# Kernel tuning notes

Measured on AMD Instinct MI355X. Metric: run time of the kernel, lower is better.

Reference implementation:

```python
import jax, jax.numpy as jnp
import numpy as np

N, H, E, P = 100000, 64, 1600000, 3


def setup_inputs() -> dict:
    key = jax.random.key(0)
    ks = jax.random.split(key, 12)
    h = jax.random.normal(ks[0], (N, H), dtype=jnp.float32)
    W = jax.random.normal(ks[1], (P, H, H), dtype=jnp.float32) * 0.1
    b = jnp.zeros((P, H), dtype=jnp.float32)
    a = jnp.full((P,), 0.25, dtype=jnp.float32)  # PReLU slopes (torch default init)
    fc_w = jax.random.normal(ks[2], (H, H), dtype=jnp.float32) * 0.1
    fc_b = jnp.zeros((H,), dtype=jnp.float32)
    att = jax.random.normal(ks[3], (H,), dtype=jnp.float32) * 0.1
    adj_vals = jax.random.uniform(ks[4], (E,), dtype=jnp.float32) * (1.0 / 16.0)
    row = jax.random.randint(ks[5], (E,), 0, N, dtype=jnp.int32)
    col = jax.random.randint(ks[6], (E,), 0, N, dtype=jnp.int32)
    mask1 = jax.random.randint(ks[7], (N,), 0, 2, dtype=jnp.int32).astype(bool)
    mask2 = jax.random.randint(ks[8], (N,), 0, 2, dtype=jnp.int32).astype(bool)
    return {"h": h, "W": W, "b": b, "a": a, "fc_w": fc_w, "fc_b": fc_b,
            "att": att, "adj_vals": adj_vals, "row": row, "col": col,
            "mask1": mask1, "mask2": mask2}


def reference(h, W, b, a, fc_w, fc_b, att, adj_vals, row, col, mask1, mask2):
    n = h.shape[0]

    def gcn_all(x):
        # P GCN layers (small fixed P): linear -> spmm(adj) -> +bias -> PReLU
        outs = []
        for p in range(W.shape[0]):
            fts = x @ W[p].T                                   # [N,H]
            msg = fts[col] * adj_vals[:, None]                  # [E,H] gather
            agg = jax.ops.segment_sum(msg, row, num_segments=n) # [N,H] scatter-add
            o = agg + b[p]
            outs.append(jnp.where(o > 0, o, a[p] * o))          # PReLU
        return jnp.stack(outs)                                  # [P,N,H]

    def attention(embeds):
        # sp_p = mean_n tanh(fc(embed_p)); beta = softmax_p(att . sp_p)
        s = jnp.tanh(jnp.einsum('pnh,kh->pnk', embeds, fc_w) + fc_b).mean(axis=1)  # [P,H]
        beta = jax.nn.softmax(s @ att, axis=0)                                      # [P]
        return jnp.einsum('pnh,p->nh', embeds, beta)                                # [N,H]

    h_masked = h * (~mask1)[:, None].astype(h.dtype)
    z_mp = attention(gcn_all(h_masked))       # encode with mask_ratio1
    z_mp2 = attention(gcn_all(h))             # encode with mask_ratio 0
    z_masked = z_mp * (~mask2)[:, None].astype(h.dtype)
    x_recon = attention(gcn_all(z_masked))    # decode
    return (z_mp, z_mp2, x_recon)
```

## Files before the change

kernel.cpp:

```cpp
#include <hip/hip_runtime.h>
#include <hip/hip_bf16.h>

typedef __hip_bfloat16 bf16;
typedef __attribute__((ext_vector_type(8))) short bf16x8;
typedef __attribute__((ext_vector_type(4))) float f32x4;


__device__ __forceinline__ short f2bf(float x) {
    unsigned u = __float_as_uint(x);
    unsigned r = (u + 0x7FFFu + ((u >> 16) & 1u)) >> 16;
    return (short)r;
}
__device__ __forceinline__ float bf2f(short s) {
    return __uint_as_float(((unsigned)(unsigned short)s) << 16);
}
__device__ __forceinline__ void split1(float v, short& h, short& l) {
    h = f2bf(v);
    l = f2bf(v - bf2f(h));
}
__device__ __forceinline__ void split1_rtz(float v, short& h, short& l) {
    unsigned u = __float_as_uint(v);
    h = (short)(u >> 16);
    float r = v - __uint_as_float(u & 0xFFFF0000u);
    l = f2bf(r);
}

__device__ __forceinline__ float fast_tanh(float x) {
    float t = __expf(x + x);
    return 1.f - __fdividef(2.f, t + 1.f);
}

__device__ __forceinline__ void fma4(float4& acc, float v, const float4& x) {
    acc.x = fmaf(v, x.x, acc.x);
    acc.y = fmaf(v, x.y, acc.y);
    acc.z = fmaf(v, x.z, acc.z);
    acc.w = fmaf(v, x.w, acc.w);
}

__device__ __forceinline__ void red4(float4& a) {
    a.x += __shfl_xor(a.x, 16); a.y += __shfl_xor(a.y, 16);
    a.z += __shfl_xor(a.z, 16); a.w += __shfl_xor(a.w, 16);
    a.x += __shfl_xor(a.x, 32); a.y += __shfl_xor(a.y, 32);
    a.z += __shfl_xor(a.z, 32); a.w += __shfl_xor(a.w, 32);
}

__global__ __launch_bounds__(256) void forensic_kernel(const unsigned int* __restrict__ mask_w,
                                                       const unsigned int* __restrict__ idx_w,
                                                       int nw_mask, int nw_idx,
                                                       int* __restrict__ flags) {
    __shared__ int sm[6];
    int t = threadIdx.x;
    if (t < 6) sm[t] = 0;
    __syncthreads();
    int m_gt1 = 0, m_f32 = 0, m_f64 = 0, m_oddnz = 0, i_hi = 0, i_oddnz = 0;
    for (int i = t; i < nw_mask; i += 256) {
        unsigned int w = mask_w[i];
        if (w > 1u && w != 0x3F800000u && w != 0x3FF00000u) m_gt1++;
        if (w == 0x3F800000u) m_f32++;
        if ((i & 1) && w == 0x3FF00000u) m_f64++;
        if ((i & 1) && w != 0u) m_oddnz++;
    }
    for (int i = t; i < nw_idx; i += 256) {
        unsigned int v = idx_w[i];
        if (v >= 0x20000000u) i_hi++;
        if ((i & 1) && v != 0u) i_oddnz++;
    }
    atomicAdd(&sm[0], m_gt1);
    atomicAdd(&sm[1], m_f32);
    atomicAdd(&sm[2], m_f64);
    atomicAdd(&sm[3], m_oddnz);
    atomicAdd(&sm[4], i_hi);
    atomicAdd(&sm[5], i_oddnz);
    __syncthreads();
    if (t == 0) {
        int mmode;
        if (sm[1] > 50) mmode = 2;
        else if (sm[2] > 50) mmode = 4;
        else if (sm[0] > 50) mmode = 0;
        else if (sm[3] > 50) mmode = 1;
        else mmode = 3;
        int imode;
        if (sm[4] > (nw_idx * 3) / 4) imode = 2;
        else if (sm[4] > nw_idx / 4) imode = 4;
        else if (sm[5] > 50) imode = 1;
        else imode = 3;
        flags[0] = mmode;
        flags[1] = imode;
    }
}

__device__ __forceinline__ int fetch_idx(const void* p, int e, int mode) {
    switch (mode) {
        case 1: return ((const int*)p)[e];
        case 3: return (int)(((const long long*)p)[e]);
        case 2: return (int)(((const float*)p)[e]);
        default: return (int)(((const double*)p)[e]);
    }
}

__device__ __forceinline__ bool conv_one(const void* m, int mode, int i) {
    switch (mode) {
        case 0: return ((const unsigned char*)m)[i] != 0;
        case 1: return ((const int*)m)[i] != 0;
        case 2: return ((const float*)m)[i] != 0.f;
        case 3: return ((const long long*)m)[i] != 0;
        default: return ((const double*)m)[i] != 0.0;
    }
}

__global__ __launch_bounds__(256) void conv_masks(const void* __restrict__ m1,
                                                  const void* __restrict__ m2,
                                                  const int* __restrict__ flags, int n,
                                                  unsigned char* __restrict__ o1,
                                                  unsigned char* __restrict__ o2) {
    int mode = flags[0];
    int i = blockIdx.x * 256 + threadIdx.x;
    if (i >= n) return;
    o1[i] = conv_one(m1, mode, i) ? 1 : 0;
    o2[i] = conv_one(m2, mode, i) ? 1 : 0;
}


__global__ __launch_bounds__(256) void split_weights(const float* __restrict__ W,
                                                     const float* __restrict__ fcw, int wn,
                                                     int fn, short* __restrict__ whi,
                                                     short* __restrict__ wlo,
                                                     short* __restrict__ fhi,
                                                     short* __restrict__ flo) {
    int i = blockIdx.x * 256 + threadIdx.x;
    if (i < wn) {
        short h, l;
        split1(W[i], h, l);
        whi[i] = h;
        wlo[i] = l;
    } else if (i < wn + fn) {
        int j = i - wn;
        short h, l;
        split1(fcw[j], h, l);
        fhi[j] = h;
        flo[j] = l;
    }
}


__global__ __launch_bounds__(256) void bucket_hist(const void* __restrict__ row,
                                                   const int* __restrict__ flags, int e_cnt,
                                                   int n, int shift, int nb,
                                                   int* __restrict__ bcnt) {
    __shared__ int hist[2048];
    int t = threadIdx.x;
    for (int i = t; i < nb; i += 256) hist[i] = 0;
    __syncthreads();
    int imode = flags[1];
    for (int e = blockIdx.x * 256 + t; e < e_cnt; e += gridDim.x * 256) {
        int r = fetch_idx(row, e, imode);
        if ((unsigned)r < (unsigned)n) atomicAdd(&hist[r >> shift], 1);
    }
    __syncthreads();
    for (int i = t; i < nb; i += 256)
        if (hist[i]) atomicAdd(&bcnt[i], hist[i]);
}

__global__ __launch_bounds__(1024) void bucket_scan(int* __restrict__ bptr, int nb,
                                                    int* __restrict__ bcur, int n,
                                                    int* __restrict__ row_ptr) {
    __shared__ int sh[1024];
    int t = threadIdx.x;
    int i0 = t * 2, i1 = t * 2 + 1;
    int a = (i0 < nb) ? bptr[i0] : 0;
    int b = (i1 < nb) ? bptr[i1] : 0;
    int s = a + b;
    sh[t] = s;
    __syncthreads();
    for (int off = 1; off < 1024; off <<= 1) {
        int u = (t >= off) ? sh[t - off] : 0;
        __syncthreads();
        sh[t] += u;
        __syncthreads();
    }
    int base = sh[t] - s;
    if (i0 < nb) { bptr[i0] = base; bcur[i0] = base; }
    if (i1 < nb) { bptr[i1] = base + a; bcur[i1] = base + a; }
    if (t == 1023) {
        bptr[nb] = sh[1023];
        row_ptr[n] = sh[1023];
    }
}

__global__ __launch_bounds__(256) void bin_pass2(const void* __restrict__ row,
                                                 const void* __restrict__ col,
                                                 const float* __restrict__ vals,
                                                 const int* __restrict__ flags, int e_cnt, int n,
                                                 int shift, int nb, int* __restrict__ bcur,
                                                 int2* __restrict__ rcbin,
                                                 float* __restrict__ valbin) {
    __shared__ int hist[2048];
    __shared__ int base[2048];
    int t = threadIdx.x;
    int e0 = blockIdx.x * 2048;
    if (e0 >= e_cnt) return;
    int imode = flags[1];
    for (int i = t; i < nb; i += 256) hist[i] = 0;
    __syncthreads();
    int rr[8], cc[8];
    float vv[8];
    bool ok[8];
#pragma unroll
    for (int j = 0; j < 8; j++) {
        int e = e0 + j * 256 + t;
        ok[j] = false;
        if (e < e_cnt) {
            int r = fetch_idx(row, e, imode);
            if ((unsigned)r < (unsigned)n) {
                ok[j] = true;
                rr[j] = r;
                int c = fetch_idx(col, e, imode);
                cc[j] = ((unsigned)c < (unsigned)n) ? c : 0;
                vv[j] = vals[e];
                atomicAdd(&hist[r >> shift], 1);
            }
        }
    }
    __syncthreads();
    for (int i = t; i < nb; i += 256) {
        int c = hist[i];
        base[i] = c ? atomicAdd(&bcur[i], c) : 0;
        hist[i] = 0;
    }
    __syncthreads();
#pragma unroll
    for (int j = 0; j < 8; j++) {
        if (ok[j]) {
            int bk = rr[j] >> shift;
            int pos = base[bk] + atomicAdd(&hist[bk], 1);
            rcbin[pos] = make_int2(rr[j], cc[j]);
            valbin[pos] = vv[j];
        }
    }
}

__global__ __launch_bounds__(512) void csr_finalize(const int* __restrict__ bptr,
                                                    const int2* __restrict__ rcbin,
                                                    const float* __restrict__ valbin, int n,
                                                    int shift, int* __restrict__ row_ptr,
                                                    int* __restrict__ col_s,
                                                    float* __restrict__ val_s) {
    __shared__ int cnt[1024];
    __shared__ int curs[1024];
    __shared__ int red[512];
    int b = blockIdx.x, t = threadIdx.x;
    int rpb = 1 << shift;
    int r0 = b << shift;
    int rows = n - r0;
    if (rows <= 0) return;
    if (rows > rpb) rows = rpb;
    int ebase = bptr[b], eend = bptr[b + 1];
    for (int i = t; i < rows; i += 512) cnt[i] = 0;
    __syncthreads();
    for (int e = ebase + t; e < eend; e += 512) atomicAdd(&cnt[rcbin[e].x - r0], 1);
    __syncthreads();
    int v[2], s = 0;
#pragma unroll
    for (int j = 0; j < 2; j++) {
        int idx = t * 2 + j;
        v[j] = (idx < rows) ? cnt[idx] : 0;
        s += v[j];
    }
    red[t] = s;
    __syncthreads();
    for (int off = 1; off < 512; off <<= 1) {
        int u = (t >= off) ? red[t - off] : 0;
        __syncthreads();
        red[t] += u;
        __syncthreads();
    }
    int run = ebase + red[t] - s;
#pragma unroll
    for (int j = 0; j < 2; j++) {
        int idx = t * 2 + j;
        if (idx < rows) {
            row_ptr[r0 + idx] = run;
            curs[idx] = run;
            run += v[j];
        }
    }
    __syncthreads();
    for (int e = ebase + t; e < eend; e += 512) {
        int2 rc = rcbin[e];
        float vv = valbin[e];
        int pos = atomicAdd(&curs[rc.x - r0], 1);
        col_s[pos] = rc.y;
        val_s[pos] = vv;
    }
}


__device__ __forceinline__ void store_split4(short* __restrict__ hi, short* __restrict__ lo,
                                             size_t o, const float4& v) {
    short4 h4, l4;
    split1(v.x, h4.x, l4.x); split1(v.y, h4.y, l4.y);
    split1(v.z, h4.z, l4.z); split1(v.w, h4.w, l4.w);
    *(short4*)(hi + o) = h4;
    *(short4*)(lo + o) = l4;
}

__global__ __launch_bounds__(256) void spmm_dual(const float* __restrict__ X,
                                                 const int* __restrict__ row_ptr,
                                                 const int* __restrict__ col_s,
                                                 const float* __restrict__ val_s,
                                                 const unsigned char* __restrict__ mask, int n,
                                                 short* __restrict__ axm_hi,
                                                 short* __restrict__ axm_lo,
                                                 short* __restrict__ axf_hi,
                                                 short* __restrict__ axf_lo) {
    int gid = blockIdx.x * 256 + threadIdx.x;
    int r = gid >> 6;
    if (r >= n) return;
    int lane = threadIdx.x & 63;
    int g = lane >> 4, sub = lane & 15;
    int s = row_ptr[r], e = row_ptr[r + 1];
    int cnt = e - s;
    int mycm = 0;
    float myv = 0.f;
    if (lane < cnt) {
        int c = col_s[s + lane];
        myv = val_s[s + lane];
        mycm = c | (mask[c] ? (1 << 30) : 0);
    }
    int cmain = cnt > 64 ? 64 : cnt;
    float4 fA = {0, 0, 0, 0}, fB = {0, 0, 0, 0};
    float4 dA = {0, 0, 0, 0}, dB = {0, 0, 0, 0};
    for (int i = 0; i < cmain; i += 16) {
        int i0 = i + g, i1 = i + 4 + g, i2 = i + 8 + g, i3 = i + 12 + g;
        int c0 = __shfl(mycm, i0), c1 = __shfl(mycm, i1);
        int c2 = __shfl(mycm, i2), c3 = __shfl(mycm, i3);
        float v0 = __shfl(myv, i0), v1 = __shfl(myv, i1);
        float v2 = __shfl(myv, i2), v3 = __shfl(myv, i3);
        if (i0 < cmain) {
            float4 x = *(const float4*)(X + (size_t)(c0 & 0x3FFFFFFF) * 64 + sub * 4);
            fma4(fA, v0, x);
            if (c0 >> 30) fma4(dA, v0, x);
        }
        if (i1 < cmain) {
            float4 x = *(const float4*)(X + (size_t)(c1 & 0x3FFFFFFF) * 64 + sub * 4);
            fma4(fB, v1, x);
            if (c1 >> 30) fma4(dB, v1, x);
        }
        if (i2 < cmain) {
            float4 x = *(const float4*)(X + (size_t)(c2 & 0x3FFFFFFF) * 64 + sub * 4);
            fma4(fA, v2, x);
            if (c2 >> 30) fma4(dA, v2, x);
        }
        if (i3 < cmain) {
            float4 x = *(const float4*)(X + (size_t)(c3 & 0x3FFFFFFF) * 64 + sub * 4);
            fma4(fB, v3, x);
            if (c3 >> 30) fma4(dB, v3, x);
        }
    }
    for (int i = 64 + g; i < cnt; i += 4) {
        int c = col_s[s + i];
        float v = val_s[s + i];
        float4 x = *(const float4*)(X + (size_t)c * 64 + sub * 4);
        fma4(fA, v, x);
        if (mask[c]) fma4(dA, v, x);
    }
    fA.x += fB.x; fA.y += fB.y; fA.z += fB.z; fA.w += fB.w;
    dA.x += dB.x; dA.y += dB.y; dA.z += dB.z; dA.w += dB.w;
    red4(fA);
    red4(dA);
    if (g == 0) {
        float4 mA = make_float4(fA.x - dA.x, fA.y - dA.y, fA.z - dA.z, fA.w - dA.w);
        size_t o = (size_t)r * 64 + sub * 4;
        store_split4(axf_hi, axf_lo, o, fA);
        store_split4(axm_hi, axm_lo, o, mA);
    }
}

__global__ __launch_bounds__(256) void spmm_one(const float* __restrict__ X,
                                                const int* __restrict__ row_ptr,
                                                const int* __restrict__ col_s,
                                                const float* __restrict__ val_s,
                                                const unsigned char* __restrict__ mask, int n,
                                                short* __restrict__ ax_hi,
                                                short* __restrict__ ax_lo) {
    int gid = blockIdx.x * 256 + threadIdx.x;
    int r = gid >> 6;
    if (r >= n) return;
    int lane = threadIdx.x & 63;
    int g = lane >> 4, sub = lane & 15;
    int s = row_ptr[r], e = row_ptr[r + 1];
    int cnt = e - s;
    int myc = 0;
    float myv = 0.f;
    if (lane < cnt) {
        myc = col_s[s + lane];
        float v = val_s[s + lane];
        myv = mask[myc] ? 0.f : v;
    }
    int cmain = cnt > 64 ? 64 : cnt;
    float4 aA = {0, 0, 0, 0}, aB = {0, 0, 0, 0};
    for (int i = 0; i < cmain; i += 16) {
        int i0 = i + g, i1 = i + 4 + g, i2 = i + 8 + g, i3 = i + 12 + g;
        int c0 = __shfl(myc, i0), c1 = __shfl(myc, i1);
        int c2 = __shfl(myc, i2), c3 = __shfl(myc, i3);
        float v0 = __shfl(myv, i0), v1 = __shfl(myv, i1);
        float v2 = __shfl(myv, i2), v3 = __shfl(myv, i3);
        if (i0 < cmain && v0 != 0.f) {
            float4 x = *(const float4*)(X + (size_t)c0 * 64 + sub * 4);
            fma4(aA, v0, x);
        }
        if (i1 < cmain && v1 != 0.f) {
            float4 x = *(const float4*)(X + (size_t)c1 * 64 + sub * 4);
            fma4(aB, v1, x);
        }
        if (i2 < cmain && v2 != 0.f) {
            float4 x = *(const float4*)(X + (size_t)c2 * 64 + sub * 4);
            fma4(aA, v2, x);
        }
        if (i3 < cmain && v3 != 0.f) {
            float4 x = *(const float4*)(X + (size_t)c3 * 64 + sub * 4);
            fma4(aB, v3, x);
        }
    }
    for (int i = 64 + g; i < cnt; i += 4) {
        int c = col_s[s + i];
        if (mask[c]) continue;
        float v = val_s[s + i];
        float4 x = *(const float4*)(X + (size_t)c * 64 + sub * 4);
        fma4(aA, v, x);
    }
    aA.x += aB.x; aA.y += aB.y; aA.z += aB.z; aA.w += aB.w;
    red4(aA);
    if (g == 0) {
        size_t o = (size_t)r * 64 + sub * 4;
        store_split4(ax_hi, ax_lo, o, aA);
    }
}


template <int PP>
__global__ __launch_bounds__(512) void gemm_tanh(const short* __restrict__ Xhi0,
                                                 const short* __restrict__ Xlo0,
                                                 const short* __restrict__ Xhi1,
                                                 const short* __restrict__ Xlo1,
                                                 const short* __restrict__ Whi_g,
                                                 const short* __restrict__ Wlo_g,
                                                 const float* __restrict__ b,
                                                 const float* __restrict__ a,
                                                 const short* __restrict__ fchi_g,
                                                 const short* __restrict__ fclo_g,
                                                 const float* __restrict__ fcb, int n, int ntiles,
                                                 float* __restrict__ s_sums) {
    __shared__ __align__(16) short ehi[2][PP][16][72], elo[2][PP][16][72];
    int set = blockIdx.y;
    const short* __restrict__ Xhi = set ? Xhi1 : Xhi0;
    const short* __restrict__ Xlo = set ? Xlo1 : Xlo0;
    float* __restrict__ ss = s_sums + set * 512;
    int t = threadIdx.x;
    int grp = t >> 8;
    int wv = (t >> 6) & 3, lane = t & 63, nl = lane & 15, q = lane >> 4;
    int colg = wv * 16 + nl;
    bf16x8 whi[PP][2], wlo[PP][2];
    float bias[PP], slope[PP];
#pragma unroll
    for (int p = 0; p < PP; p++) {
#pragma unroll
        for (int kk = 0; kk < 2; kk++) {
            whi[p][kk] = *(const bf16x8*)(Whi_g + p * 4096 + colg * 64 + kk * 32 + q * 8);
            wlo[p][kk] = *(const bf16x8*)(Wlo_g + p * 4096 + colg * 64 + kk * 32 + q * 8);
        }
        bias[p] = b[p * 64 + colg];
        slope[p] = a[p];
    }
    bf16x8 fhi[2], flo[2];
#pragma unroll
    for (int kk = 0; kk < 2; kk++) {
        fhi[kk] = *(const bf16x8*)(fchi_g + colg * 64 + kk * 32 + q * 8);
        flo[kk] = *(const bf16x8*)(fclo_g + colg * 64 + kk * 32 + q * 8);
    }
    float fbias = fcb[colg];
    float ssum[PP];
#pragma unroll
    for (int p = 0; p < PP; p++) ssum[p] = 0.f;

    int npairs = (ntiles + 1) >> 1;
    int pi = blockIdx.x;
    int rt = pi * 2 + grp;
    bool act = rt < ntiles;
    bf16x8 ah[2], al[2];
    if (act) {
        size_t rb = (size_t)(rt * 16 + nl) * 64 + q * 8;
#pragma unroll
        for (int kk = 0; kk < 2; kk++) {
            ah[kk] = *(const bf16x8*)(Xhi + rb + kk * 32);
            al[kk] = *(const bf16x8*)(Xlo + rb + kk * 32);
        }
    }
    for (; pi < npairs; pi += gridDim.x) {
        rt = pi * 2 + grp;
        act = rt < ntiles;
        if (act) {
#pragma unroll
            for (int p = 0; p < PP; p++) {
                f32x4 acc = {0.f, 0.f, 0.f, 0.f};
                acc = __builtin_amdgcn_mfma_f32_16x16x32_bf16(ah[0], whi[p][0], acc, 0, 0, 0);
                acc = __builtin_amdgcn_mfma_f32_16x16x32_bf16(ah[1], whi[p][1], acc, 0, 0, 0);
                acc = __builtin_amdgcn_mfma_f32_16x16x32_bf16(al[0], whi[p][0], acc, 0, 0, 0);
                acc = __builtin_amdgcn_mfma_f32_16x16x32_bf16(al[1], whi[p][1], acc, 0, 0, 0);
                acc = __builtin_amdgcn_mfma_f32_16x16x32_bf16(ah[0], wlo[p][0], acc, 0, 0, 0);
                acc = __builtin_amdgcn_mfma_f32_16x16x32_bf16(ah[1], wlo[p][1], acc, 0, 0, 0);
                acc = __builtin_amdgcn_mfma_f32_16x16x32_bf16(al[0], wlo[p][0], acc, 0, 0, 0);
                acc = __builtin_amdgcn_mfma_f32_16x16x32_bf16(al[1], wlo[p][1], acc, 0, 0, 0);
#pragma unroll
                for (int i = 0; i < 4; i++) {
                    float o = acc[i] + bias[p];
                    o = (o > 0.f) ? o : slope[p] * o;
                    short hb, lb;
                    split1_rtz(o, hb, lb);
                    ehi[grp][p][q * 4 + i][colg] = hb;
                    elo[grp][p][q * 4 + i][colg] = lb;
                }
            }
        }
        int pn = pi + gridDim.x;
        int rn = pn * 2 + grp;
        bf16x8 pfh[2], pfl[2];
        if (pn < npairs && rn < ntiles) {
            size_t rb = (size_t)(rn * 16 + nl) * 64 + q * 8;
#pragma unroll
            for (int kk = 0; kk < 2; kk++) {
                pfh[kk] = *(const bf16x8*)(Xhi + rb + kk * 32);
                pfl[kk] = *(const bf16x8*)(Xlo + rb + kk * 32);
            }
        }
        __syncthreads();
        if (act) {
#pragma unroll
            for (int p = 0; p < PP; p++) {
                bf16x8 eh[2], el[2];
#pragma unroll
                for (int kk = 0; kk < 2; kk++) {
                    eh[kk] = *(const bf16x8*)(&ehi[grp][p][nl][kk * 32 + q * 8]);
                    el[kk] = *(const bf16x8*)(&elo[grp][p][nl][kk * 32 + q * 8]);
                }
                f32x4 acc = {0.f, 0.f, 0.f, 0.f};
                acc = __builtin_amdgcn_mfma_f32_16x16x32_bf16(eh[0], fhi[0], acc, 0, 0, 0);
                acc = __builtin_amdgcn_mfma_f32_16x16x32_bf16(eh[1], fhi[1], acc, 0, 0, 0);
                acc = __builtin_amdgcn_mfma_f32_16x16x32_bf16(el[0], fhi[0], acc, 0, 0, 0);
                acc = __builtin_amdgcn_mfma_f32_16x16x32_bf16(el[1], fhi[1], acc, 0, 0, 0);
                acc = __builtin_amdgcn_mfma_f32_16x16x32_bf16(eh[0], flo[0], acc, 0, 0, 0);
                acc = __builtin_amdgcn_mfma_f32_16x16x32_bf16(eh[1], flo[1], acc, 0, 0, 0);
#pragma unroll
                for (int i = 0; i < 4; i++) {
                    int r = rt * 16 + q * 4 + i;
                    if (r < n) ssum[p] += fast_tanh(acc[i] + fbias);
                }
            }
        }
        __syncthreads();
#pragma unroll
        for (int kk = 0; kk < 2; kk++) {
            ah[kk] = pfh[kk];
            al[kk] = pfl[kk];
        }
    }
#pragma unroll
    for (int p = 0; p < PP; p++) {
        float s = ssum[p];
        s += __shfl_xor(s, 16);
        s += __shfl_xor(s, 32);
        if (q == 0) atomicAdd(&ss[p * 64 + colg], s);
    }
}


template <int PP>
__global__ __launch_bounds__(256) void gemm_mix(const short* __restrict__ Xhi0,
                                                const short* __restrict__ Xlo0,
                                                const short* __restrict__ Xhi1,
                                                const short* __restrict__ Xlo1,
                                                const short* __restrict__ Whi_g,
                                                const short* __restrict__ Wlo_g,
                                                const float* __restrict__ b,
                                                const float* __restrict__ a,
                                                const float* __restrict__ beta, int n, int ntiles,
                                                float* __restrict__ outbase, int accum) {
    int set = blockIdx.y;
    const short* __restrict__ Xhi = set ? Xhi1 : Xhi0;
    const short* __restrict__ Xlo = set ? Xlo1 : Xlo0;
    float* __restrict__ out = outbase + (size_t)set * n * 64;
    int t = threadIdx.x;
    int wv = t >> 6, lane = t & 63, nl = lane & 15, q = lane >> 4;
    int colg = wv * 16 + nl;
    bf16x8 whi[PP][2], wlo[PP][2];
    float bias[PP], slope[PP], bet[PP];
#pragma unroll
    for (int p = 0; p < PP; p++) {
#pragma unroll
        for (int kk = 0; kk < 2; kk++) {
            whi[p][kk] = *(const bf16x8*)(Whi_g + p * 4096 + colg * 64 + kk * 32 + q * 8);
            wlo[p][kk] = *(const bf16x8*)(Wlo_g + p * 4096 + colg * 64 + kk * 32 + q * 8);
        }
        bias[p] = b[p * 64 + colg];
        slope[p] = a[p];
        bet[p] = beta[set * 8 + p];
    }
    int rt = blockIdx.x;
    bf16x8 ah[2], al[2];
    if (rt < ntiles) {
        size_t rb = (size_t)(rt * 16 + nl) * 64 + q * 8;
#pragma unroll
        for (int kk = 0; kk < 2; kk++) {
            ah[kk] = *(const bf16x8*)(Xhi + rb + kk * 32);
            al[kk] = *(const bf16x8*)(Xlo + rb + kk * 32);
        }
    }
    for (; rt < ntiles; rt += gridDim.x) {
        int rn = rt + gridDim.x;
        bf16x8 pfh[2], pfl[2];
        if (rn < ntiles) {
            size_t rb = (size_t)(rn * 16 + nl) * 64 + q * 8;
#pragma unroll
            for (int kk = 0; kk < 2; kk++) {
                pfh[kk] = *(const bf16x8*)(Xhi + rb + kk * 32);
                pfl[kk] = *(const bf16x8*)(Xlo + rb + kk * 32);
            }
        }
        float mix[4] = {0.f, 0.f, 0.f, 0.f};
#pragma unroll
        for (int p = 0; p < PP; p++) {
            f32x4 acc = {0.f, 0.f, 0.f, 0.f};
            acc = __builtin_amdgcn_mfma_f32_16x16x32_bf16(ah[0], whi[p][0], acc, 0, 0, 0);
            acc = __builtin_amdgcn_mfma_f32_16x16x32_bf16(ah[1], whi[p][1], acc, 0, 0, 0);
            acc = __builtin_amdgcn_mfma_f32_16x16x32_bf16(al[0], whi[p][0], acc, 0, 0, 0);
            acc = __builtin_amdgcn_mfma_f32_16x16x32_bf16(al[1], whi[p][1], acc, 0, 0, 0);
            acc = __builtin_amdgcn_mfma_f32_16x16x32_bf16(ah[0], wlo[p][0], acc, 0, 0, 0);
            acc = __builtin_amdgcn_mfma_f32_16x16x32_bf16(ah[1], wlo[p][1], acc, 0, 0, 0);
            acc = __builtin_amdgcn_mfma_f32_16x16x32_bf16(al[0], wlo[p][0], acc, 0, 0, 0);
            acc = __builtin_amdgcn_mfma_f32_16x16x32_bf16(al[1], wlo[p][1], acc, 0, 0, 0);
#pragma unroll
            for (int i = 0; i < 4; i++) {
                float o = acc[i] + bias[p];
                o = (o > 0.f) ? o : slope[p] * o;
                mix[i] = fmaf(bet[p], o, mix[i]);
            }
        }
#pragma unroll
        for (int i = 0; i < 4; i++) {
            int r = rt * 16 + q * 4 + i;
            if (r < n) {
                size_t idx = (size_t)r * 64 + colg;
                out[idx] = accum ? (out[idx] + mix[i]) : mix[i];
            }
        }
#pragma unroll
        for (int kk = 0; kk < 2; kk++) {
            ah[kk] = pfh[kk];
            al[kk] = pfl[kk];
        }
    }
}

__global__ __launch_bounds__(64) void compute_beta(const float* __restrict__ s_sums,
                                                   const float* __restrict__ att, int n, int P,
                                                   int nsets, float* __restrict__ beta) {
    int lane = threadIdx.x;
    float av = att[lane];
    for (int st = 0; st < nsets; st++) {
        const float* ss = s_sums + st * 512;
        float l[8];
        for (int p = 0; p < P; p++) l[p] = ss[p * 64 + lane] * av;
#pragma unroll
        for (int off = 32; off > 0; off >>= 1)
            for (int p = 0; p < 8; p++)
                if (p < P) l[p] += __shfl_down(l[p], off);
        if (lane == 0) {
            const float inv = 1.0f / (float)n;
            float m = -1e30f;
            for (int p = 0; p < P; p++) {
                l[p] *= inv;
                m = fmaxf(m, l[p]);
            }
            float s = 0.f;
            for (int p = 0; p < P; p++) {
                l[p] = __expf(l[p] - m);
                s += l[p];
            }
            for (int p = 0; p < P; p++) beta[st * 8 + p] = l[p] / s;
        }
    }
}


extern "C" void kernel_launch(void* const* d_in, const int* in_sizes, int n_in,
                              void* d_out, int out_size, void* d_ws, size_t ws_size,
                              hipStream_t stream) {
    const float* h = (const float*)d_in[0];
    const float* W = (const float*)d_in[1];
    const float* b = (const float*)d_in[2];
    const float* a = (const float*)d_in[3];
    const float* fc_w = (const float*)d_in[4];
    const float* fc_b = (const float*)d_in[5];
    const float* att = (const float*)d_in[6];
    const float* adj = (const float*)d_in[7];
    const void* row = d_in[8];
    const void* col = d_in[9];
    const void* mask1 = d_in[10];
    const void* mask2 = d_in[11];
    float* out = (float*)d_out;

    int P = in_sizes[3];
    if (P < 1 || P > 8) P = 3;
    int N = in_sizes[0] / 64;
    int E = in_sizes[7];
    int N16 = (N + 15) & ~15;
    int ntiles = N16 >> 4;

    int shift = 8;
    while (((N >> shift) + 1) > 2048) shift++;
    int NB = (N >> shift) + 1;

    char* w = (char*)d_ws;
    auto alloc = [&](size_t bytes) {
        void* p = (void*)w;
        w += (bytes + 255) & ~(size_t)255;
        return p;
    };
    int* row_ptr = (int*)alloc((size_t)(N + 1) * 4);
    int* col_s = (int*)alloc((size_t)E * 4);
    float* val_s = (float*)alloc((size_t)E * 4);
    int* bptr = (int*)alloc((size_t)(NB + 1) * 4);
    int* bcur = (int*)alloc((size_t)NB * 4);
    int2* rcbin = (int2*)alloc((size_t)E * 8);
    float* valbin = (float*)alloc((size_t)E * 4);
    unsigned char* m1c = (unsigned char*)alloc(N);
    unsigned char* m2c = (unsigned char*)alloc(N);
    short* axm_hi = (short*)alloc((size_t)N16 * 64 * 2);
    short* axm_lo = (short*)alloc((size_t)N16 * 64 * 2);
    short* axf_hi = (short*)alloc((size_t)N16 * 64 * 2);
    short* axf_lo = (short*)alloc((size_t)N16 * 64 * 2);
    short* whi_g = (short*)alloc((size_t)8 * 4096 * 2);
    short* wlo_g = (short*)alloc((size_t)8 * 4096 * 2);
    short* fchi_g = (short*)alloc((size_t)4096 * 2);
    short* fclo_g = (short*)alloc((size_t)4096 * 2);
    float* s_sums = (float*)alloc(2 * 512 * 4);
    float* beta = (float*)alloc(64 * 4);
    int* flags = (int*)alloc(256);

    int nw_mask = N / 4 > 25000 ? 25000 : N / 4;
    int nw_idx = E / 4 > 25000 ? 25000 : E / 4;
    forensic_kernel<<<1, 256, 0, stream>>>((const unsigned int*)mask1, (const unsigned int*)row,
                                           nw_mask, nw_idx, flags);
    conv_masks<<<(N + 255) / 256, 256, 0, stream>>>(mask1, mask2, flags, N, m1c, m2c);
    int wn = P * 4096, fn = 4096;
    split_weights<<<(wn + fn + 255) / 256, 256, 0, stream>>>(W, fc_w, wn, fn, whi_g, wlo_g,
                                                            fchi_g, fclo_g);

    hipMemsetAsync(bptr, 0, (size_t)(NB + 1) * 4, stream);
    if (N16 > N) {
        size_t padoff = (size_t)N * 64, padbytes = (size_t)(N16 - N) * 64 * 2;
        hipMemsetAsync(axm_hi + padoff, 0, padbytes, stream);
        hipMemsetAsync(axm_lo + padoff, 0, padbytes, stream);
        hipMemsetAsync(axf_hi + padoff, 0, padbytes, stream);
        hipMemsetAsync(axf_lo + padoff, 0, padbytes, stream);
    }
    bucket_hist<<<1024, 256, 0, stream>>>(row, flags, E, N, shift, NB, bptr);
    bucket_scan<<<1, 1024, 0, stream>>>(bptr, NB, bcur, N, row_ptr);
    int bin_blocks = (E + 2047) / 2048;
    bin_pass2<<<bin_blocks, 256, 0, stream>>>(row, col, adj, flags, E, N, shift, NB, bcur, rcbin,
                                              valbin);
    csr_finalize<<<NB, 512, 0, stream>>>(bptr, rcbin, valbin, N, shift, row_ptr, col_s, val_s);

    int spmm_grid = (int)(((size_t)N * 64 + 255) / 256);
    int tanh_blocks = 1024;
    int mix_blocks = 1024;

    auto tail = [&](const short* xh0, const short* xl0, const short* xh1, const short* xl1,
                    int nsets, float* dst) {
        hipMemsetAsync(s_sums, 0, 2 * 512 * 4, stream);
        if (P == 3) {
            gemm_tanh<3><<<dim3(tanh_blocks, nsets), 512, 0, stream>>>(
                xh0, xl0, xh1, xl1, whi_g, wlo_g, b, a, fchi_g, fclo_g, fc_b, N, ntiles, s_sums);
        } else {
            for (int p = 0; p < P; p++)
                gemm_tanh<1><<<dim3(tanh_blocks, nsets), 512, 0, stream>>>(
                    xh0, xl0, xh1, xl1, whi_g + p * 4096, wlo_g + p * 4096, b + p * 64, a + p,
                    fchi_g, fclo_g, fc_b, N, ntiles, s_sums + p * 64);
        }
        compute_beta<<<1, 64, 0, stream>>>(s_sums, att, N, P, nsets, beta);
        if (P == 3) {
            gemm_mix<3><<<dim3(mix_blocks, nsets), 256, 0, stream>>>(
                xh0, xl0, xh1, xl1, whi_g, wlo_g, b, a, beta, N, ntiles, dst, 0);
        } else {
            for (int p = 0; p < P; p++)
                gemm_mix<1><<<dim3(mix_blocks, nsets), 256, 0, stream>>>(
                    xh0, xl0, xh1, xl1, whi_g + p * 4096, wlo_g + p * 4096, b + p * 64, a + p,
                    beta + p, N, ntiles, dst, p != 0);
        }
    };

    spmm_dual<<<spmm_grid, 256, 0, stream>>>(h, row_ptr, col_s, val_s, m1c, N, axm_hi, axm_lo,
                                             axf_hi, axf_lo);
    tail(axm_hi, axm_lo, axf_hi, axf_lo, 2, out);
    spmm_one<<<spmm_grid, 256, 0, stream>>>(out, row_ptr, col_s, val_s, m2c, N, axm_hi, axm_lo);
    tail(axm_hi, axm_lo, axm_hi, axm_lo, 1, out + (size_t)2 * N * 64);
}
```

Before: 647.5 us.

## Software-pipeline gemm_tanh with double-buffered LDS and one barrier per tile

After: 573.9 us. 11.4% less time.

```diff
diff --git a/kernel.cpp b/kernel.cpp
--- a/kernel.cpp
+++ b/kernel.cpp
@@ -439,7 +439,7 @@
 
 
 template <int PP>
-__global__ __launch_bounds__(512) void gemm_tanh(const short* __restrict__ Xhi0,
+__global__ __launch_bounds__(256) void gemm_tanh(const short* __restrict__ Xhi0,
                                                  const short* __restrict__ Xlo0,
                                                  const short* __restrict__ Xhi1,
                                                  const short* __restrict__ Xlo1,
@@ -457,8 +457,7 @@
     const short* __restrict__ Xlo = set ? Xlo1 : Xlo0;
     float* __restrict__ ss = s_sums + set * 512;
     int t = threadIdx.x;
-    int grp = t >> 8;
-    int wv = (t >> 6) & 3, lane = t & 63, nl = lane & 15, q = lane >> 4;
+    int wv = t >> 6, lane = t & 63, nl = lane & 15, q = lane >> 4;
     int colg = wv * 16 + nl;
     bf16x8 whi[PP][2], wlo[PP][2];
     float bias[PP], slope[PP];
@@ -483,86 +482,77 @@
 #pragma unroll
     for (int p = 0; p < PP; p++) ssum[p] = 0.f;
 
-    int npairs = (ntiles + 1) >> 1;
-    int pi = blockIdx.x;
-    int rt = pi * 2 + grp;
-    bool act = rt < ntiles;
-    bf16x8 ah[2], al[2];
-    if (act) {
+    int G = gridDim.x;
+    int rt0 = blockIdx.x;
+    if (rt0 >= ntiles) return;
+
+    auto loadA = [&](int rt, bf16x8 xh[2], bf16x8 xl[2]) {
         size_t rb = (size_t)(rt * 16 + nl) * 64 + q * 8;
 #pragma unroll
         for (int kk = 0; kk < 2; kk++) {
-            ah[kk] = *(const bf16x8*)(Xhi + rb + kk * 32);
-            al[kk] = *(const bf16x8*)(Xlo + rb + kk * 32);
-        }
-    }
-    for (; pi < npairs; pi += gridDim.x) {
-        rt = pi * 2 + grp;
-        act = rt < ntiles;
-        if (act) {
-#pragma unroll
-            for (int p = 0; p < PP; p++) {
-                f32x4 acc = {0.f, 0.f, 0.f, 0.f};
-                acc = __builtin_amdgcn_mfma_f32_16x16x32_bf16(ah[0], whi[p][0], acc, 0, 0, 0);
-                acc = __builtin_amdgcn_mfma_f32_16x16x32_bf16(ah[1], whi[p][1], acc, 0, 0, 0);
-                acc = __builtin_amdgcn_mfma_f32_16x16x32_bf16(al[0], whi[p][0], acc, 0, 0, 0);
-                acc = __builtin_amdgcn_mfma_f32_16x16x32_bf16(al[1], whi[p][1], acc, 0, 0, 0);
-                acc = __builtin_amdgcn_mfma_f32_16x16x32_bf16(ah[0], wlo[p][0], acc, 0, 0, 0);
-                acc = __builtin_amdgcn_mfma_f32_16x16x32_bf16(ah[1], wlo[p][1], acc, 0, 0, 0);
-                acc = __builtin_amdgcn_mfma_f32_16x16x32_bf16(al[0], wlo[p][0], acc, 0, 0, 0);
-                acc = __builtin_amdgcn_mfma_f32_16x16x32_bf16(al[1], wlo[p][1], acc, 0, 0, 0);
-#pragma unroll
-                for (int i = 0; i < 4; i++) {
-                    float o = acc[i] + bias[p];
-                    o = (o > 0.f) ? o : slope[p] * o;
-                    short hb, lb;
-                    split1_rtz(o, hb, lb);
-                    ehi[grp][p][q * 4 + i][colg] = hb;
-                    elo[grp][p][q * 4 + i][colg] = lb;
-                }
-            }
-        }
-        int pn = pi + gridDim.x;
-        int rn = pn * 2 + grp;
-        bf16x8 pfh[2], pfl[2];
-        if (pn < npairs && rn < ntiles) {
-            size_t rb = (size_t)(rn * 16 + nl) * 64 + q * 8;
+            xh[kk] = *(const bf16x8*)(Xhi + rb + kk * 32);
+            xl[kk] = *(const bf16x8*)(Xlo + rb + kk * 32);
+        }
+    };
+    auto embed = [&](bf16x8 xh[2], bf16x8 xl[2], int bsel) {
+#pragma unroll
+        for (int p = 0; p < PP; p++) {
+            f32x4 acc = {0.f, 0.f, 0.f, 0.f};
+            acc = __builtin_amdgcn_mfma_f32_16x16x32_bf16(xh[0], whi[p][0], acc, 0, 0, 0);
+            acc = __builtin_amdgcn_mfma_f32_16x16x32_bf16(xh[1], whi[p][1], acc, 0, 0, 0);
+            acc = __builtin_amdgcn_mfma_f32_16x16x32_bf16(xl[0], whi[p][0], acc, 0, 0, 0);
+            acc = __builtin_amdgcn_mfma_f32_16x16x32_bf16(xl[1], whi[p][1], acc, 0, 0, 0);
+            acc = __builtin_amdgcn_mfma_f32_16x16x32_bf16(xh[0], wlo[p][0], acc, 0, 0, 0);
+            acc = __builtin_amdgcn_mfma_f32_16x16x32_bf16(xh[1], wlo[p][1], acc, 0, 0, 0);
+            acc = __builtin_amdgcn_mfma_f32_16x16x32_bf16(xl[0], wlo[p][0], acc, 0, 0, 0);
+            acc = __builtin_amdgcn_mfma_f32_16x16x32_bf16(xl[1], wlo[p][1], acc, 0, 0, 0);
+#pragma unroll
+            for (int i = 0; i < 4; i++) {
+                float o = acc[i] + bias[p];
+                o = (o > 0.f) ? o : slope[p] * o;
+                short hb, lb;
+                split1_rtz(o, hb, lb);
+                ehi[bsel][p][q * 4 + i][colg] = hb;
+                elo[bsel][p][q * 4 + i][colg] = lb;
+            }
+        }
+    };
+
+    bf16x8 ah[2], al[2], pfh[2], pfl[2];
+    loadA(rt0, ah, al);
+    embed(ah, al, 0);
+    if (rt0 + G < ntiles) loadA(rt0 + G, pfh, pfl);
+
+    int buf = 0;
+    for (int rt = rt0; rt < ntiles; rt += G) {
+        int rn = rt + G;
+        __syncthreads();
+        if (rn < ntiles) {
+            embed(pfh, pfl, buf ^ 1);
+            if (rn + G < ntiles) loadA(rn + G, pfh, pfl);
+        }
+#pragma unroll
+        for (int p = 0; p < PP; p++) {
+            bf16x8 eh[2], el[2];
 #pragma unroll
             for (int kk = 0; kk < 2; kk++) {
-                pfh[kk] = *(const bf16x8*)(Xhi + rb + kk * 32);
-                pfl[kk] = *(const bf16x8*)(Xlo + rb + kk * 32);
-            }
-        }
-        __syncthreads();
-        if (act) {
-#pragma unroll
-            for (int p = 0; p < PP; p++) {
-                bf16x8 eh[2], el[2];
-#pragma unroll
-                for (int kk = 0; kk < 2; kk++) {
-                    eh[kk] = *(const bf16x8*)(&ehi[grp][p][nl][kk * 32 + q * 8]);
-                    el[kk] = *(const bf16x8*)(&elo[grp][p][nl][kk * 32 + q * 8]);
-                }
-                f32x4 acc = {0.f, 0.f, 0.f, 0.f};
-                acc = __builtin_amdgcn_mfma_f32_16x16x32_bf16(eh[0], fhi[0], acc, 0, 0, 0);
-                acc = __builtin_amdgcn_mfma_f32_16x16x32_bf16(eh[1], fhi[1], acc, 0, 0, 0);
-                acc = __builtin_amdgcn_mfma_f32_16x16x32_bf16(el[0], fhi[0], acc, 0, 0, 0);
-                acc = __builtin_amdgcn_mfma_f32_16x16x32_bf16(el[1], fhi[1], acc, 0, 0, 0);
-                acc = __builtin_amdgcn_mfma_f32_16x16x32_bf16(eh[0], flo[0], acc, 0, 0, 0);
-                acc = __builtin_amdgcn_mfma_f32_16x16x32_bf16(eh[1], flo[1], acc, 0, 0, 0);
-#pragma unroll
-                for (int i = 0; i < 4; i++) {
-                    int r = rt * 16 + q * 4 + i;
-                    if (r < n) ssum[p] += fast_tanh(acc[i] + fbias);
-                }
-            }
-        }
-        __syncthreads();
-#pragma unroll
-        for (int kk = 0; kk < 2; kk++) {
-            ah[kk] = pfh[kk];
-            al[kk] = pfl[kk];
-        }
+                eh[kk] = *(const bf16x8*)(&ehi[buf][p][nl][kk * 32 + q * 8]);
+                el[kk] = *(const bf16x8*)(&elo[buf][p][nl][kk * 32 + q * 8]);
+            }
+            f32x4 acc = {0.f, 0.f, 0.f, 0.f};
+            acc = __builtin_amdgcn_mfma_f32_16x16x32_bf16(eh[0], fhi[0], acc, 0, 0, 0);
+            acc = __builtin_amdgcn_mfma_f32_16x16x32_bf16(eh[1], fhi[1], acc, 0, 0, 0);
+            acc = __builtin_amdgcn_mfma_f32_16x16x32_bf16(el[0], fhi[0], acc, 0, 0, 0);
+            acc = __builtin_amdgcn_mfma_f32_16x16x32_bf16(el[1], fhi[1], acc, 0, 0, 0);
+            acc = __builtin_amdgcn_mfma_f32_16x16x32_bf16(eh[0], flo[0], acc, 0, 0, 0);
+            acc = __builtin_amdgcn_mfma_f32_16x16x32_bf16(eh[1], flo[1], acc, 0, 0, 0);
+#pragma unroll
+            for (int i = 0; i < 4; i++) {
+                int r = rt * 16 + q * 4 + i;
+                if (r < n) ssum[p] += fast_tanh(acc[i] + fbias);
+            }
+        }
+        buf ^= 1;
     }
 #pragma unroll
     for (int p = 0; p < PP; p++) {
@@ -779,11 +769,11 @@
                     int nsets, float* dst) {
         hipMemsetAsync(s_sums, 0, 2 * 512 * 4, stream);
         if (P == 3) {
-            gemm_tanh<3><<<dim3(tanh_blocks, nsets), 512, 0, stream>>>(
+            gemm_tanh<3><<<dim3(tanh_blocks, nsets), 256, 0, stream>>>(
                 xh0, xl0, xh1, xl1, whi_g, wlo_g, b, a, fchi_g, fclo_g, fc_b, N, ntiles, s_sums);
         } else {
             for (int p = 0; p < P; p++)
-                gemm_tanh<1><<<dim3(tanh_blocks, nsets), 512, 0, stream>>>(
+                gemm_tanh<1><<<dim3(tanh_blocks, nsets), 256, 0, stream>>>(
                     xh0, xl0, xh1, xl1, whi_g + p * 4096, wlo_g + p * 4096, b + p * 64, a + p,
                     fchi_g, fclo_g, fc_b, N, ntiles, s_sums + p * 64);
         }
```
